# Kernel tuning notes

Measured on AMD Instinct MI355X. Metric: run time of the kernel, lower is better.

The kernel has to match this reference:

```python
import jax, jax.numpy as jnp
import numpy as np

B = 8192
C, S1, S2 = 3, 64, 64
F = C * S1 * S2          # 12288 flattened input features
SU = 4096                # s_units
HID = 1024               # hidden_size
NL = 4                   # s_layers
D = 8                    # num_domains
H1, H2, NW = 28, 14, 5   # omniglot head dims, num_ways
BN_EPS = 1e-5
LEAK = 0.001


def setup_inputs() -> dict:
    key = jax.random.key(0)
    ks = jax.random.split(key, 24)
    sc = 0.02
    n = lambda k, shp: (jax.random.normal(k, shp, jnp.float32) * sc)
    return {
        'x_s': jax.random.normal(ks[0], (B, C, S1, S2), jnp.float32),
        'x_p': jax.random.normal(ks[1], (B, C, S1, S2), jnp.float32),
        'tt': jax.random.randint(ks[2], (B,), 0, D),
        'domain_id': 3,
        # Shared MLP
        'W_in': n(ks[3], (F, SU)),  'b_in': jnp.zeros((SU,), jnp.float32),
        'W_hid': n(ks[4], (SU, SU)), 'b_hid': jnp.zeros((SU,), jnp.float32),
        'W_out': n(ks[5], (SU, HID)), 'b_out': jnp.zeros((HID,), jnp.float32),
        # Private per-domain linear (stacked)
        'Wp': n(ks[6], (D, F, HID)), 'bp': jnp.zeros((D, HID), jnp.float32),
        # BatchNorm1d affine params
        'gamma': jnp.ones((2 * HID,), jnp.float32),
        'beta': jnp.zeros((2 * HID,), jnp.float32),
        # Per-domain head MLPs (stacked)
        'Wh1': n(ks[7], (D, 2 * HID, H1)), 'bh1': jnp.zeros((D, H1), jnp.float32),
        'Wh2': n(ks[8], (D, H1, H2)),      'bh2': jnp.zeros((D, H2), jnp.float32),
        'Wh3': n(ks[9], (D, H2, NW)),      'bh3': jnp.zeros((D, NW), jnp.float32),
    }


def _forward(x_s, x_p, tt, domain_id, W_in, b_in, W_hid, b_hid, W_out, b_out,
             Wp, bp, gamma, beta, Wh1, bh1, Wh2, bh2, Wh3, bh3):
    b = x_s.shape[0]
    hs = x_s.reshape(b, -1)
    hp = x_p.reshape(b, -1)

    # Shared branch (dropout = identity in eval)
    h = jax.nn.relu(hs @ W_in + b_in)
    for _ in range(NL):
        h = jax.nn.relu(h @ W_hid + b_hid)
    h_shared = jax.nn.relu(h @ W_out + b_out)

    # Private branch: single domain-selected linear + LeakyReLU(0.001)
    h_priv = jax.nn.leaky_relu(hp @ Wp[domain_id] + bp[domain_id], LEAK)

    x = jnp.concatenate([h_shared, h_priv], axis=1)  # [B, 2*HID]

    # BatchNorm1d (training-mode batch statistics, biased variance)
    mean = jnp.mean(x, axis=0)
    var = jnp.var(x, axis=0)
    x = (x - mean) * jax.lax.rsqrt(var + BN_EPS) * gamma + beta

    # Per-sample task-routed heads: gather weights by tt, batched GEMMs
    y = jax.nn.relu(jnp.einsum('bf,bfo->bo', x, Wh1[tt]) + bh1[tt])
    y = jax.nn.relu(jnp.einsum('bf,bfo->bo', y, Wh2[tt]) + bh2[tt])
    y = jnp.einsum('bf,bfo->bo', y, Wh3[tt]) + bh3[tt]
    return y  # [B, num_ways]


def reference(x_s, x_p, tt, domain_id, W_in, b_in, W_hid, b_hid, W_out, b_out,
              Wp, bp, gamma, beta, Wh1, bh1, Wh2, bh2, Wh3, bh3):
    return _forward(x_s, x_p, tt, domain_id, W_in, b_in, W_hid, b_hid,
                    W_out, b_out, Wp, bp, gamma, beta,
                    Wh1, bh1, Wh2, bh2, Wh3, bh3)
```

## Files before the change

### kernel.cpp

```cpp
#include <hip/hip_runtime.h>
#include <hip/hip_bf16.h>

#define BQ    8192
#define FIN   12288
#define SUN   4096
#define HIDN  1024
#define XW    2048
#define H1N   28
#define H2N   14
#define NWAY  5
#define BN_EPS 1e-5f
#define LEAKS 0.001f

typedef __bf16 bf16x8 __attribute__((ext_vector_type(8)));
typedef float  f32x4  __attribute__((ext_vector_type(4)));
typedef unsigned short ushort8 __attribute__((ext_vector_type(8)));

__device__ __forceinline__ unsigned short f2bf(float f) {
    unsigned u = __float_as_uint(f);
    unsigned r = u + 0x7fffu + ((u >> 16) & 1u);
    return (unsigned short)(r >> 16);
}

__device__ __forceinline__ ushort8 cvt8(const float4 a, const float4 b) {
    union { __bf16 h[8]; ushort8 u; } r;
    r.h[0] = (__bf16)a.x; r.h[1] = (__bf16)a.y;
    r.h[2] = (__bf16)a.z; r.h[3] = (__bf16)a.w;
    r.h[4] = (__bf16)b.x; r.h[5] = (__bf16)b.y;
    r.h[6] = (__bf16)b.z; r.h[7] = (__bf16)b.w;
    return r.u;
}

#define TO_LDS(p) ((__attribute__((address_space(3))) void*)(p))
#define TO_GLB(p) ((const __attribute__((address_space(1))) void*)(p))


__global__ __launch_bounds__(256) void cvt_bf16(
    const float* __restrict__ in, unsigned short* __restrict__ out, long long n8)
{
    const long long idx = (long long)blockIdx.x * 256 + threadIdx.x;
    const long long stride = (long long)gridDim.x * 256;
    for (long long i = idx; i < n8; i += stride) {
        const float4 a = ((const float4*)in)[2 * i];
        const float4 b = ((const float4*)in)[2 * i + 1];
        ((ushort8*)out)[i] = cvt8(a, b);
    }
}

__global__ __launch_bounds__(256) void transpose_cvt(
    const float* __restrict__ in, unsigned short* __restrict__ out,
    int R, int Cc, const int* __restrict__ dom)
{
    if (dom) in += (size_t)(*dom) * (size_t)R * (size_t)Cc;
    __shared__ float tile[64][65];
    const int t  = threadIdx.x;
    const int tr = t >> 4;
    const int tc = t & 15;
    const int c0 = blockIdx.x * 64;
    const int r0 = blockIdx.y * 64;

    #pragma unroll
    for (int q = 0; q < 4; ++q) {
        const int r = r0 + tr + q * 16;
        const float4 v = *(const float4*)&in[(size_t)r * Cc + c0 + tc * 4];
        tile[tc*4+0][tr + q*16] = v.x;
        tile[tc*4+1][tr + q*16] = v.y;
        tile[tc*4+2][tr + q*16] = v.z;
        tile[tc*4+3][tr + q*16] = v.w;
    }
    __syncthreads();
    #pragma unroll
    for (int q = 0; q < 4; ++q) {
        const int c = c0 + tr + q * 16;
        ushort4 o;
        o.x = f2bf(tile[tr + q*16][tc*4+0]);
        o.y = f2bf(tile[tr + q*16][tc*4+1]);
        o.z = f2bf(tile[tr + q*16][tc*4+2]);
        o.w = f2bf(tile[tr + q*16][tc*4+3]);
        *(ushort4*)&out[(size_t)c * R + r0 + tc * 4] = o;
    }
}

template<bool A_F32, bool OUT_F32, int ACT>
__global__ __launch_bounds__(256) void gemm_mfma(
    const void* __restrict__ Ap, const unsigned short* __restrict__ Bt,
    const float* __restrict__ bias, void* __restrict__ Cp,
    int M, int N, int K, int ldc, int cc0,
    const int* __restrict__ dom, int biasStride)
{
    __shared__ alignas(16) unsigned short As[128 * 32];
    __shared__ alignas(16) unsigned short Bs[128 * 32];

    const int nbx = N >> 7;
    int wg = blockIdx.x;
    const int nwg = gridDim.x;
    if ((nwg & 7) == 0) {
        const int cpx = nwg >> 3;
        wg = (wg & 7) * cpx + (wg >> 3);
    }
    const int bx = wg % nbx, by = wg / nbx;
    const int row0 = by << 7, col0 = bx << 7;

    const int t  = threadIdx.x;
    const int w  = t >> 6;
    const int l  = t & 63;
    const int wr = w >> 1, wc = w & 1;
    const int lr = l & 15, lk = l >> 4;
    const int rsw = (lr >> 1) & 3;

    f32x4 acc[4][4];
    #pragma unroll
    for (int i = 0; i < 4; ++i)
        #pragma unroll
        for (int j = 0; j < 4; ++j)
            acc[i][j] = (f32x4)(0.f);

    const int srow = l >> 2;
    const int skb  = (((l & 3) ^ ((l >> 3) & 3)) * 16);
    const float* Af = (const float*)Ap;
    const unsigned short* Ab = (const unsigned short*)Ap;

    for (int k0 = 0; k0 < K; k0 += 32) {
        __syncthreads();

        #pragma unroll
        for (int c = 0; c < 2; ++c) {
            const int inst = w * 2 + c;
            const int row  = inst * 16 + srow;
            const char* src = (const char*)Bt +
                (((size_t)(col0 + row) * K + k0) * 2 + skb);
            char* dst = (char*)Bs + inst * 1024;
            __builtin_amdgcn_global_load_lds(TO_GLB(src), TO_LDS(dst), 16, 0, 0);
        }
        if (!A_F32) {
            #pragma unroll
            for (int c = 0; c < 2; ++c) {
                const int inst = w * 2 + c;
                const int row  = inst * 16 + srow;
                const char* src = (const char*)Ab +
                    (((size_t)(row0 + row) * K + k0) * 2 + skb);
                char* dst = (char*)As + inst * 1024;
                __builtin_amdgcn_global_load_lds(TO_GLB(src), TO_LDS(dst), 16, 0, 0);
            }
        } else {
            #pragma unroll
            for (int c = 0; c < 2; ++c) {
                const int ci  = t + 256 * c;
                const int row = ci >> 2;
                const int ko  = (((ci & 3) ^ ((ci >> 3) & 3)) * 8);
                const float* s = Af + (size_t)(row0 + row) * K + k0 + ko;
                const float4 v0 = *(const float4*)s;
                const float4 v1 = *(const float4*)(s + 4);
                *(ushort8*)&As[ci * 8] = cvt8(v0, v1);
            }
        }
        __syncthreads();

        bf16x8 af[4], bfv[4];
        #pragma unroll
        for (int i = 0; i < 4; ++i)
            af[i]  = *(const bf16x8*)&As[(wr*64 + i*16 + lr) * 32 + (lk ^ rsw) * 8];
        #pragma unroll
        for (int j = 0; j < 4; ++j)
            bfv[j] = *(const bf16x8*)&Bs[(wc*64 + j*16 + lr) * 32 + (lk ^ rsw) * 8];
        #pragma unroll
        for (int i = 0; i < 4; ++i)
            #pragma unroll
            for (int j = 0; j < 4; ++j)
                acc[i][j] = __builtin_amdgcn_mfma_f32_16x16x32_bf16(
                    af[i], bfv[j], acc[i][j], 0, 0, 0);
    }

    if (dom) bias += (*dom) * biasStride;
    const int colb = col0 + wc * 64 + lr;
    const int rowb = row0 + wr * 64 + lk * 4;
    float bj[4];
    #pragma unroll
    for (int j = 0; j < 4; ++j) bj[j] = bias[colb + j * 16];

    #pragma unroll
    for (int i = 0; i < 4; ++i) {
        #pragma unroll
        for (int r = 0; r < 4; ++r) {
            const size_t row = rowb + i * 16 + r;
            #pragma unroll
            for (int j = 0; j < 4; ++j) {
                float x = acc[i][j][r] + bj[j];
                if (ACT == 1)      x = fmaxf(x, 0.f);
                else if (ACT == 2) x = (x > 0.f) ? x : LEAKS * x;
                const size_t idx = row * (size_t)ldc + cc0 + colb + j * 16;
                if (OUT_F32) ((float*)Cp)[idx] = x;
                else         ((unsigned short*)Cp)[idx] = f2bf(x);
            }
        }
    }
}

__global__ __launch_bounds__(512, 2) void gemm256(
    const unsigned short* __restrict__ A, const unsigned short* __restrict__ Bt,
    const float* __restrict__ bias, unsigned short* __restrict__ C,
    int M, int N, int K)
{
    __shared__ alignas(16) unsigned short lds[3][2][256 * 32];

    const int nbx = N >> 8;
    int wg = blockIdx.x;
    const int nwg = gridDim.x;
    if ((nwg & 7) == 0) {
        const int cpx = nwg >> 3;
        wg = (wg & 7) * cpx + (wg >> 3);
    }
    const int bx = wg % nbx, by = wg / nbx;
    const int row0 = by << 8, col0 = bx << 8;

    const int t  = threadIdx.x;
    const int w  = t >> 6, l = t & 63;
    const int wr = w >> 2, wc = w & 3;
    const int lr = l & 15, lk = l >> 4;
    const int rsw = (lr >> 1) & 3;
    const int srow = l >> 2;
    const int skel = ((l & 3) ^ ((l >> 3) & 3)) * 8;

    f32x4 acc[8][4];
    #pragma unroll
    for (int i = 0; i < 8; ++i)
        #pragma unroll
        for (int j = 0; j < 4; ++j)
            acc[i][j] = (f32x4)(0.f);

    const int NT = K >> 5;

    #define STAGE256(tile_)  do {                                            \
        const int k0_  = (tile_) << 5;                                       \
        const int buf_ = (tile_) % 3;                                        \
        _Pragma("unroll")                                                    \
        for (int s_ = 0; s_ < 2; ++s_) {                                     \
            const int c_   = w * 2 + s_;                                     \
            const int row_ = c_ * 16 + srow;                                 \
            __builtin_amdgcn_global_load_lds(                                \
                TO_GLB(A + (size_t)(row0 + row_) * K + k0_ + skel),          \
                TO_LDS((char*)&lds[buf_][0][0] + c_ * 1024), 16, 0, 0);      \
            __builtin_amdgcn_global_load_lds(                                \
                TO_GLB(Bt + (size_t)(col0 + row_) * K + k0_ + skel),         \
                TO_LDS((char*)&lds[buf_][1][0] + c_ * 1024), 16, 0, 0);      \
        }                                                                    \
    } while (0)

    STAGE256(0);
    if (NT > 1) {
        STAGE256(1);
        asm volatile("s_waitcnt vmcnt(4)" ::: "memory");
    } else {
        asm volatile("s_waitcnt vmcnt(0)" ::: "memory");
    }
    __builtin_amdgcn_sched_barrier(0);
    __builtin_amdgcn_s_barrier();
    __builtin_amdgcn_sched_barrier(0);

    for (int tt = 0; tt < NT; ++tt) {
        const int buf = tt % 3;
        if (tt + 2 < NT) STAGE256(tt + 2);
        __builtin_amdgcn_sched_barrier(0);

        bf16x8 af[8], bfv[4];
        #pragma unroll
        for (int i = 0; i < 8; ++i)
            af[i]  = *(const bf16x8*)&lds[buf][0][(wr*128 + i*16 + lr) * 32 + (lk ^ rsw) * 8];
        #pragma unroll
        for (int j = 0; j < 4; ++j)
            bfv[j] = *(const bf16x8*)&lds[buf][1][(wc*64 + j*16 + lr) * 32 + (lk ^ rsw) * 8];

        __builtin_amdgcn_s_setprio(1);
        #pragma unroll
        for (int j = 0; j < 4; ++j)
            #pragma unroll
            for (int i = 0; i < 8; ++i)
                acc[i][j] = __builtin_amdgcn_mfma_f32_16x16x32_bf16(
                    af[i], bfv[j], acc[i][j], 0, 0, 0);
        __builtin_amdgcn_s_setprio(0);

        if (tt + 1 < NT) {
            if (tt + 2 < NT) asm volatile("s_waitcnt vmcnt(4)" ::: "memory");
            else             asm volatile("s_waitcnt vmcnt(0)" ::: "memory");
            __builtin_amdgcn_sched_barrier(0);
            __builtin_amdgcn_s_barrier();
            __builtin_amdgcn_sched_barrier(0);
        }
    }
    #undef STAGE256

    const int colb = col0 + wc * 64 + lr;
    const int rowb = row0 + wr * 128 + lk * 4;
    float bj[4];
    #pragma unroll
    for (int j = 0; j < 4; ++j) bj[j] = bias[colb + j * 16];

    #pragma unroll
    for (int i = 0; i < 8; ++i) {
        #pragma unroll
        for (int r = 0; r < 4; ++r) {
            const size_t row = rowb + i * 16 + r;
            #pragma unroll
            for (int j = 0; j < 4; ++j) {
                float x = fmaxf(acc[i][j][r] + bj[j], 0.f);
                C[row * (size_t)N + colb + j * 16] = f2bf(x);
            }
        }
    }
}

template<bool OUT_F32, int ACT>
__global__ __launch_bounds__(256, 2) void gemm128(
    const unsigned short* __restrict__ A, const unsigned short* __restrict__ Bt,
    const float* __restrict__ bias, void* __restrict__ Cp,
    int M, int N, int K, int ldc, int cc0,
    const int* __restrict__ dom, int biasStride)
{
    __shared__ alignas(16) unsigned short lds[3][2][128 * 32];

    const int nbx = N >> 7;
    int wg = blockIdx.x;
    const int nwg = gridDim.x;
    if ((nwg & 7) == 0) {
        const int cpx = nwg >> 3;
        wg = (wg & 7) * cpx + (wg >> 3);
    }
    const int bx = wg % nbx, by = wg / nbx;
    const int row0 = by << 7, col0 = bx << 7;

    const int t  = threadIdx.x;
    const int w  = t >> 6, l = t & 63;
    const int wr = w >> 1, wc = w & 1;
    const int lr = l & 15, lk = l >> 4;
    const int rsw = (lr >> 1) & 3;
    const int srow = l >> 2;
    const int skel = ((l & 3) ^ ((l >> 3) & 3)) * 8;

    f32x4 acc[4][4];
    #pragma unroll
    for (int i = 0; i < 4; ++i)
        #pragma unroll
        for (int j = 0; j < 4; ++j)
            acc[i][j] = (f32x4)(0.f);

    const int NT = K >> 5;

    #define STAGE128(tile_)  do {                                            \
        const int k0_  = (tile_) << 5;                                       \
        const int buf_ = (tile_) % 3;                                        \
        _Pragma("unroll")                                                    \
        for (int s_ = 0; s_ < 2; ++s_) {                                     \
            const int c_   = w * 2 + s_;                                     \
            const int row_ = c_ * 16 + srow;                                 \
            __builtin_amdgcn_global_load_lds(                                \
                TO_GLB(A + (size_t)(row0 + row_) * K + k0_ + skel),          \
                TO_LDS((char*)&lds[buf_][0][0] + c_ * 1024), 16, 0, 0);      \
            __builtin_amdgcn_global_load_lds(                                \
                TO_GLB(Bt + (size_t)(col0 + row_) * K + k0_ + skel),         \
                TO_LDS((char*)&lds[buf_][1][0] + c_ * 1024), 16, 0, 0);      \
        }                                                                    \
    } while (0)

    STAGE128(0);
    if (NT > 1) {
        STAGE128(1);
        asm volatile("s_waitcnt vmcnt(4)" ::: "memory");
    } else {
        asm volatile("s_waitcnt vmcnt(0)" ::: "memory");
    }
    __builtin_amdgcn_sched_barrier(0);
    __builtin_amdgcn_s_barrier();
    __builtin_amdgcn_sched_barrier(0);

    for (int tt = 0; tt < NT; ++tt) {
        const int buf = tt % 3;
        if (tt + 2 < NT) STAGE128(tt + 2);
        __builtin_amdgcn_sched_barrier(0);

        bf16x8 af[4], bfv[4];
        #pragma unroll
        for (int i = 0; i < 4; ++i)
            af[i]  = *(const bf16x8*)&lds[buf][0][(wr*64 + i*16 + lr) * 32 + (lk ^ rsw) * 8];
        #pragma unroll
        for (int j = 0; j < 4; ++j)
            bfv[j] = *(const bf16x8*)&lds[buf][1][(wc*64 + j*16 + lr) * 32 + (lk ^ rsw) * 8];

        #pragma unroll
        for (int j = 0; j < 4; ++j)
            #pragma unroll
            for (int i = 0; i < 4; ++i)
                acc[i][j] = __builtin_amdgcn_mfma_f32_16x16x32_bf16(
                    af[i], bfv[j], acc[i][j], 0, 0, 0);

        if (tt + 1 < NT) {
            if (tt + 2 < NT) asm volatile("s_waitcnt vmcnt(4)" ::: "memory");
            else             asm volatile("s_waitcnt vmcnt(0)" ::: "memory");
            __builtin_amdgcn_sched_barrier(0);
            __builtin_amdgcn_s_barrier();
            __builtin_amdgcn_sched_barrier(0);
        }
    }
    #undef STAGE128

    if (dom) bias += (*dom) * biasStride;
    const int colb = col0 + wc * 64 + lr;
    const int rowb = row0 + wr * 64 + lk * 4;
    float bj[4];
    #pragma unroll
    for (int j = 0; j < 4; ++j) bj[j] = bias[colb + j * 16];

    #pragma unroll
    for (int i = 0; i < 4; ++i) {
        #pragma unroll
        for (int r = 0; r < 4; ++r) {
            const size_t row = rowb + i * 16 + r;
            #pragma unroll
            for (int j = 0; j < 4; ++j) {
                float x = acc[i][j][r] + bj[j];
                if (ACT == 1)      x = fmaxf(x, 0.f);
                else if (ACT == 2) x = (x > 0.f) ? x : LEAKS * x;
                const size_t idx = row * (size_t)ldc + cc0 + colb + j * 16;
                if (OUT_F32) ((float*)Cp)[idx] = x;
                else         ((unsigned short*)Cp)[idx] = f2bf(x);
            }
        }
    }
}

__global__ __launch_bounds__(256) void bn_stats_a(
    const float* __restrict__ X, float* __restrict__ psum, float* __restrict__ pss)
{
    const int c  = blockIdx.x * 256 + threadIdx.x;
    const int rb = blockIdx.y;
    float s = 0.f, ss = 0.f;
    const int r0 = rb * 256;
    for (int r = r0; r < r0 + 256; ++r) {
        float v = X[(size_t)r * XW + c];
        s += v; ss = fmaf(v, v, ss);
    }
    psum[rb * XW + c] = s;
    pss [rb * XW + c] = ss;
}

__global__ __launch_bounds__(256) void bn_stats_b(
    const float* __restrict__ psum, const float* __restrict__ pss,
    const float* __restrict__ gamma, const float* __restrict__ beta,
    float* __restrict__ scale, float* __restrict__ shift)
{
    const int c = blockIdx.x * 256 + threadIdx.x;
    float s = 0.f, ss = 0.f;
    for (int rb = 0; rb < 32; ++rb) { s += psum[rb * XW + c]; ss += pss[rb * XW + c]; }
    const float inv = 1.f / (float)BQ;
    const float mean = s * inv;
    const float var  = ss * inv - mean * mean;
    const float sc = gamma[c] * rsqrtf(var + BN_EPS);
    scale[c] = sc;
    shift[c] = beta[c] - mean * sc;
}

__global__ __launch_bounds__(256) void head_kernel(
    const float* __restrict__ X, const float* __restrict__ scale,
    const float* __restrict__ shift, const int* __restrict__ tt,
    const float* __restrict__ Wh1, const float* __restrict__ bh1,
    const float* __restrict__ Wh2, const float* __restrict__ bh2,
    const float* __restrict__ Wh3, const float* __restrict__ bh3,
    float* __restrict__ out)
{
    __shared__ float xs[4][XW];
    __shared__ float y1[4][H1N];
    __shared__ float y2[4][H2N + 2];

    const int t = threadIdx.x;
    const int w = t >> 6;
    const int l = t & 63;
    const int s = blockIdx.x * 4 + w;
    const int d = tt[s];

    #pragma unroll 4
    for (int i = 0; i < XW / 64; ++i) {
        const int c = i * 64 + l;
        xs[w][c] = fmaf(X[(size_t)s * XW + c], scale[c], shift[c]);
    }
    __syncthreads();

    if (l < H1N) {
        const float* W1 = Wh1 + (size_t)d * XW * H1N;
        float acc = bh1[d * H1N + l];
        #pragma unroll 8
        for (int c = 0; c < XW; ++c)
            acc = fmaf(xs[w][c], W1[c * H1N + l], acc);
        y1[w][l] = fmaxf(acc, 0.f);
    }
    __syncthreads();

    if (l < H2N) {
        const float* W2 = Wh2 + (size_t)d * H1N * H2N;
        float acc = bh2[d * H2N + l];
        #pragma unroll
        for (int c = 0; c < H1N; ++c)
            acc = fmaf(y1[w][c], W2[c * H2N + l], acc);
        y2[w][l] = fmaxf(acc, 0.f);
    }
    __syncthreads();

    if (l < NWAY) {
        const float* W3 = Wh3 + (size_t)d * H2N * NWAY;
        float acc = bh3[d * NWAY + l];
        #pragma unroll
        for (int c = 0; c < H2N; ++c)
            acc = fmaf(y2[w][c], W3[c * NWAY + l], acc);
        out[(size_t)s * NWAY + l] = acc;
    }
}

extern "C" void kernel_launch(void* const* d_in, const int* in_sizes, int n_in,
                              void* d_out, int out_size, void* d_ws, size_t ws_size,
                              hipStream_t stream)
{
    const float* x_s   = (const float*)d_in[0];
    const float* x_p   = (const float*)d_in[1];
    const int*   tt    = (const int*)  d_in[2];
    const int*   dom   = (const int*)  d_in[3];
    const float* W_in  = (const float*)d_in[4];
    const float* b_in  = (const float*)d_in[5];
    const float* W_hid = (const float*)d_in[6];
    const float* b_hid = (const float*)d_in[7];
    const float* W_out = (const float*)d_in[8];
    const float* b_out = (const float*)d_in[9];
    const float* Wp    = (const float*)d_in[10];
    const float* bp    = (const float*)d_in[11];
    const float* gamma = (const float*)d_in[12];
    const float* beta  = (const float*)d_in[13];
    const float* Wh1   = (const float*)d_in[14];
    const float* bh1   = (const float*)d_in[15];
    const float* Wh2   = (const float*)d_in[16];
    const float* bh2   = (const float*)d_in[17];
    const float* Wh3   = (const float*)d_in[18];
    const float* bh3   = (const float*)d_in[19];
    float* out = (float*)d_out;

    const dim3 blk(256);
    char* w = (char*)d_ws;

    const size_t FAST_NEED = 470810624ull;

    if (ws_size >= FAST_NEED) {
        unsigned short* xb    = (unsigned short*)w;
        unsigned short* WinT  = (unsigned short*)(w + 201326592);
        unsigned short* WoutT = (unsigned short*)(w + 201326592);
        unsigned short* WpT   = (unsigned short*)(w + 209715200);
        unsigned short* actA  = (unsigned short*)(w + 301989888);
        unsigned short* actB  = (unsigned short*)(w + 369098752);
        float*          X     = (float*)(w + 369098752);
        unsigned short* WhidT = (unsigned short*)(w + 436207616);
        float*          psum  = (float*)(w + 469762048);
        float*          pss   = psum + 32 * XW;
        float*          scale = pss  + 32 * XW;
        float*          shift = scale + XW;

        cvt_bf16<<<dim3(2048), blk, 0, stream>>>(x_s, xb, (long long)BQ * FIN / 8);
        transpose_cvt<<<dim3(SUN/64,  FIN/64), blk, 0, stream>>>(W_in,  WinT,  FIN, SUN,  nullptr);
        transpose_cvt<<<dim3(SUN/64,  SUN/64), blk, 0, stream>>>(W_hid, WhidT, SUN, SUN,  nullptr);

        gemm256<<<dim3(512), dim3(512), 0, stream>>>(xb, WinT, b_in, actA, BQ, SUN, FIN);

        transpose_cvt<<<dim3(HIDN/64, SUN/64), blk, 0, stream>>>(W_out, WoutT, SUN, HIDN, nullptr);
        transpose_cvt<<<dim3(HIDN/64, FIN/64), blk, 0, stream>>>(Wp,    WpT,   FIN, HIDN, dom);
        cvt_bf16<<<dim3(2048), blk, 0, stream>>>(x_p, xb, (long long)BQ * FIN / 8);

        gemm256<<<dim3(512), dim3(512), 0, stream>>>(actA, WhidT, b_hid, actB, BQ, SUN, SUN);
        gemm256<<<dim3(512), dim3(512), 0, stream>>>(actB, WhidT, b_hid, actA, BQ, SUN, SUN);
        gemm256<<<dim3(512), dim3(512), 0, stream>>>(actA, WhidT, b_hid, actB, BQ, SUN, SUN);
        gemm256<<<dim3(512), dim3(512), 0, stream>>>(actB, WhidT, b_hid, actA, BQ, SUN, SUN);

        gemm128<true,1><<<dim3(512), blk, 0, stream>>>(
            actA, WoutT, b_out, X, BQ, HIDN, SUN, XW, 0, nullptr, 0);
        gemm128<true,2><<<dim3(512), blk, 0, stream>>>(
            xb, WpT, bp, X, BQ, HIDN, FIN, XW, HIDN, dom, HIDN);

        bn_stats_a<<<dim3(XW/256, 32), blk, 0, stream>>>(X, psum, pss);
        bn_stats_b<<<dim3(XW/256),     blk, 0, stream>>>(psum, pss, gamma, beta, scale, shift);
        head_kernel<<<dim3(BQ/4), blk, 0, stream>>>(X, scale, shift, tt,
                                                    Wh1, bh1, Wh2, bh2, Wh3, bh3, out);
        return;
    }

    unsigned short* actA  = (unsigned short*)w;
    unsigned short* actB  = (unsigned short*)(w + 67108864);
    float*          X     = (float*)(w + 67108864);
    unsigned short* WinT  = (unsigned short*)(w + 134217728);
    unsigned short* WoutT = (unsigned short*)(w + 134217728);
    unsigned short* WpT   = (unsigned short*)(w + 142606336);
    float*          psum  = (float*)(w + 167772160);
    float*          pss   = psum + 32 * XW;
    float*          scale = pss  + 32 * XW;
    float*          shift = scale + XW;
    unsigned short* WhidT = (unsigned short*)(w + 234881024);

    transpose_cvt<<<dim3(SUN/64,  FIN/64), blk, 0, stream>>>(W_in,  WinT,  FIN, SUN,  nullptr);
    transpose_cvt<<<dim3(SUN/64,  SUN/64), blk, 0, stream>>>(W_hid, WhidT, SUN, SUN,  nullptr);

    gemm_mfma<true,false,1><<<dim3(2048), blk, 0, stream>>>(
        x_s, WinT, b_in, actA, BQ, SUN, FIN, SUN, 0, nullptr, 0);

    transpose_cvt<<<dim3(HIDN/64, SUN/64), blk, 0, stream>>>(W_out, WoutT, SUN, HIDN, nullptr);
    transpose_cvt<<<dim3(HIDN/64, FIN/64), blk, 0, stream>>>(Wp,    WpT,   FIN, HIDN, dom);

    gemm256<<<dim3(512), dim3(512), 0, stream>>>(actA, WhidT, b_hid, actB, BQ, SUN, SUN);
    gemm256<<<dim3(512), dim3(512), 0, stream>>>(actB, WhidT, b_hid, actA, BQ, SUN, SUN);
    gemm256<<<dim3(512), dim3(512), 0, stream>>>(actA, WhidT, b_hid, actB, BQ, SUN, SUN);
    gemm256<<<dim3(512), dim3(512), 0, stream>>>(actB, WhidT, b_hid, actA, BQ, SUN, SUN);

    gemm128<true,1><<<dim3(512), blk, 0, stream>>>(
        actA, WoutT, b_out, X, BQ, HIDN, SUN, XW, 0, nullptr, 0);
    gemm_mfma<true,true,2><<<dim3(512), blk, 0, stream>>>(
        x_p, WpT, bp, X, BQ, HIDN, FIN, XW, HIDN, dom, HIDN);

    bn_stats_a<<<dim3(XW/256, 32), blk, 0, stream>>>(X, psum, pss);
    bn_stats_b<<<dim3(XW/256),     blk, 0, stream>>>(psum, pss, gamma, beta, scale, shift);
    head_kernel<<<dim3(BQ/4), blk, 0, stream>>>(X, scale, shift, tt,
                                                Wh1, bh1, Wh2, bh2, Wh3, bh3, out);
}
```

Before: 2.521 ms.

## Rework 256x256 GEMM to BK=64 double buffer with phased MFMA scheduling

Replaces the 3-stage BK=32 LDS pipeline with a 2-stage BK=64 double buffer using an XOR swizzle over 8 chunks. The inner loop is split into four quadrant phases that interleave LDS reads with MFMAs. An optional PHASED variant adds workgroup barriers around each phase so waves issue their MFMA bursts together, and it is applied to alternating hidden-layer GEMMs. The aim is fewer barriers per K and better LDS/MFMA overlap. The cost is that each prefetch now waits on vmcnt(0), so there is less latency hiding, and LDS usage per block rises to 128KB.

```diff
diff --git a/kernel.cpp b/kernel.cpp
--- a/kernel.cpp
+++ b/kernel.cpp
@@ -34,7 +34,6 @@
 #define TO_LDS(p) ((__attribute__((address_space(3))) void*)(p))
 #define TO_GLB(p) ((const __attribute__((address_space(1))) void*)(p))
 
-
 __global__ __launch_bounds__(256) void cvt_bf16(
     const float* __restrict__ in, unsigned short* __restrict__ out, long long n8)
 {
@@ -196,12 +195,14 @@
     }
 }
 
-__global__ __launch_bounds__(512, 2) void gemm256(
+template<bool PHASED>
+__global__ __launch_bounds__(512, 2) void gemm256v2(
     const unsigned short* __restrict__ A, const unsigned short* __restrict__ Bt,
     const float* __restrict__ bias, unsigned short* __restrict__ C,
     int M, int N, int K)
 {
-    __shared__ alignas(16) unsigned short lds[3][2][256 * 32];
+    __shared__ alignas(16) unsigned short As[2][256 * 64];
+    __shared__ alignas(16) unsigned short Bs[2][256 * 64];
 
     const int nbx = N >> 8;
     int wg = blockIdx.x;
@@ -217,9 +218,6 @@
     const int w  = t >> 6, l = t & 63;
     const int wr = w >> 2, wc = w & 3;
     const int lr = l & 15, lk = l >> 4;
-    const int rsw = (lr >> 1) & 3;
-    const int srow = l >> 2;
-    const int skel = ((l & 3) ^ ((l >> 3) & 3)) * 8;
 
     f32x4 acc[8][4];
     #pragma unroll
@@ -228,66 +226,86 @@
         for (int j = 0; j < 4; ++j)
             acc[i][j] = (f32x4)(0.f);
 
-    const int NT = K >> 5;
-
-    #define STAGE256(tile_)  do {                                            \
-        const int k0_  = (tile_) << 5;                                       \
-        const int buf_ = (tile_) % 3;                                        \
-        _Pragma("unroll")                                                    \
-        for (int s_ = 0; s_ < 2; ++s_) {                                     \
-            const int c_   = w * 2 + s_;                                     \
-            const int row_ = c_ * 16 + srow;                                 \
-            __builtin_amdgcn_global_load_lds(                                \
-                TO_GLB(A + (size_t)(row0 + row_) * K + k0_ + skel),          \
-                TO_LDS((char*)&lds[buf_][0][0] + c_ * 1024), 16, 0, 0);      \
-            __builtin_amdgcn_global_load_lds(                                \
-                TO_GLB(Bt + (size_t)(col0 + row_) * K + k0_ + skel),         \
-                TO_LDS((char*)&lds[buf_][1][0] + c_ * 1024), 16, 0, 0);      \
-        }                                                                    \
+    const int NT = K >> 6;
+
+    #define STAGEV2(tile_)  do {                                              \
+        const int k0_ = (tile_) << 6;                                         \
+        const int b_  = (tile_) & 1;                                          \
+        _Pragma("unroll")                                                     \
+        for (int h_ = 0; h_ < 2; ++h_)                                        \
+        _Pragma("unroll")                                                     \
+        for (int s_ = 0; s_ < 2; ++s_) {                                      \
+            const int ch_  = h_ * 1024 + s_ * 512 + t;                        \
+            const int row_ = ch_ >> 3;                                        \
+            const int g_   = (ch_ & 7) ^ (row_ & 7);                          \
+            __builtin_amdgcn_global_load_lds(                                 \
+                TO_GLB(A + (size_t)(row0 + row_) * K + k0_ + g_ * 8),         \
+                TO_LDS((char*)&As[b_][0] + ch_ * 16), 16, 0, 0);              \
+            __builtin_amdgcn_global_load_lds(                                 \
+                TO_GLB(Bt + (size_t)(col0 + row_) * K + k0_ + g_ * 8),        \
+                TO_LDS((char*)&Bs[b_][0] + ch_ * 16), 16, 0, 0);              \
+        }                                                                     \
     } while (0)
 
-    STAGE256(0);
-    if (NT > 1) {
-        STAGE256(1);
-        asm volatile("s_waitcnt vmcnt(4)" ::: "memory");
-    } else {
-        asm volatile("s_waitcnt vmcnt(0)" ::: "memory");
-    }
+    STAGEV2(0);
+    asm volatile("s_waitcnt vmcnt(0)" ::: "memory");
     __builtin_amdgcn_sched_barrier(0);
     __builtin_amdgcn_s_barrier();
     __builtin_amdgcn_sched_barrier(0);
 
     for (int tt = 0; tt < NT; ++tt) {
-        const int buf = tt % 3;
-        if (tt + 2 < NT) STAGE256(tt + 2);
+        const int b = tt & 1;
+        if (tt + 1 < NT) STAGEV2(tt + 1);
         __builtin_amdgcn_sched_barrier(0);
 
-        bf16x8 af[8], bfv[4];
-        #pragma unroll
-        for (int i = 0; i < 8; ++i)
-            af[i]  = *(const bf16x8*)&lds[buf][0][(wr*128 + i*16 + lr) * 32 + (lk ^ rsw) * 8];
-        #pragma unroll
-        for (int j = 0; j < 4; ++j)
-            bfv[j] = *(const bf16x8*)&lds[buf][1][(wc*64 + j*16 + lr) * 32 + (lk ^ rsw) * 8];
-
-        __builtin_amdgcn_s_setprio(1);
-        #pragma unroll
-        for (int j = 0; j < 4; ++j)
-            #pragma unroll
-            for (int i = 0; i < 8; ++i)
-                acc[i][j] = __builtin_amdgcn_mfma_f32_16x16x32_bf16(
-                    af[i], bfv[j], acc[i][j], 0, 0, 0);
-        __builtin_amdgcn_s_setprio(0);
+        #pragma unroll
+        for (int ph = 0; ph < 4; ++ph) {
+            const int qi = ph >> 1, qj = ph & 1;
+
+            bf16x8 av[2][4], bv[2][2];
+            #pragma unroll
+            for (int ks = 0; ks < 2; ++ks)
+                #pragma unroll
+                for (int i = 0; i < 4; ++i) {
+                    const int row = wr * 128 + qi * 64 + i * 16 + lr;
+                    av[ks][i] = *(const bf16x8*)
+                        &As[b][row * 64 + (((ks * 4 + lk) ^ (row & 7)) << 3)];
+                }
+            #pragma unroll
+            for (int ks = 0; ks < 2; ++ks)
+                #pragma unroll
+                for (int j = 0; j < 2; ++j) {
+                    const int row = wc * 64 + qj * 32 + j * 16 + lr;
+                    bv[ks][j] = *(const bf16x8*)
+                        &Bs[b][row * 64 + (((ks * 4 + lk) ^ (row & 7)) << 3)];
+                }
+
+            if (PHASED) {
+                __builtin_amdgcn_s_barrier();
+                asm volatile("s_waitcnt lgkmcnt(0)" ::: "memory");
+                __builtin_amdgcn_sched_barrier(0);
+            }
+            __builtin_amdgcn_s_setprio(1);
+            #pragma unroll
+            for (int ks = 0; ks < 2; ++ks)
+                #pragma unroll
+                for (int j = 0; j < 2; ++j)
+                    #pragma unroll
+                    for (int i = 0; i < 4; ++i)
+                        acc[qi*4+i][qj*2+j] = __builtin_amdgcn_mfma_f32_16x16x32_bf16(
+                            av[ks][i], bv[ks][j], acc[qi*4+i][qj*2+j], 0, 0, 0);
+            __builtin_amdgcn_s_setprio(0);
+            if (PHASED) __builtin_amdgcn_s_barrier();
+        }
 
         if (tt + 1 < NT) {
-            if (tt + 2 < NT) asm volatile("s_waitcnt vmcnt(4)" ::: "memory");
-            else             asm volatile("s_waitcnt vmcnt(0)" ::: "memory");
+            asm volatile("s_waitcnt vmcnt(0)" ::: "memory");
             __builtin_amdgcn_sched_barrier(0);
             __builtin_amdgcn_s_barrier();
             __builtin_amdgcn_sched_barrier(0);
         }
     }
-    #undef STAGE256
+    #undef STAGEV2
 
     const int colb = col0 + wc * 64 + lr;
     const int rowb = row0 + wr * 128 + lk * 4;
@@ -562,16 +580,16 @@
         transpose_cvt<<<dim3(SUN/64,  FIN/64), blk, 0, stream>>>(W_in,  WinT,  FIN, SUN,  nullptr);
         transpose_cvt<<<dim3(SUN/64,  SUN/64), blk, 0, stream>>>(W_hid, WhidT, SUN, SUN,  nullptr);
 
-        gemm256<<<dim3(512), dim3(512), 0, stream>>>(xb, WinT, b_in, actA, BQ, SUN, FIN);
+        gemm256v2<false><<<dim3(512), dim3(512), 0, stream>>>(xb, WinT, b_in, actA, BQ, SUN, FIN);
 
         transpose_cvt<<<dim3(HIDN/64, SUN/64), blk, 0, stream>>>(W_out, WoutT, SUN, HIDN, nullptr);
         transpose_cvt<<<dim3(HIDN/64, FIN/64), blk, 0, stream>>>(Wp,    WpT,   FIN, HIDN, dom);
         cvt_bf16<<<dim3(2048), blk, 0, stream>>>(x_p, xb, (long long)BQ * FIN / 8);
 
-        gemm256<<<dim3(512), dim3(512), 0, stream>>>(actA, WhidT, b_hid, actB, BQ, SUN, SUN);
-        gemm256<<<dim3(512), dim3(512), 0, stream>>>(actB, WhidT, b_hid, actA, BQ, SUN, SUN);
-        gemm256<<<dim3(512), dim3(512), 0, stream>>>(actA, WhidT, b_hid, actB, BQ, SUN, SUN);
-        gemm256<<<dim3(512), dim3(512), 0, stream>>>(actB, WhidT, b_hid, actA, BQ, SUN, SUN);
+        gemm256v2<false><<<dim3(512), dim3(512), 0, stream>>>(actA, WhidT, b_hid, actB, BQ, SUN, SUN);
+        gemm256v2<true ><<<dim3(512), dim3(512), 0, stream>>>(actB, WhidT, b_hid, actA, BQ, SUN, SUN);
+        gemm256v2<false><<<dim3(512), dim3(512), 0, stream>>>(actA, WhidT, b_hid, actB, BQ, SUN, SUN);
+        gemm256v2<true ><<<dim3(512), dim3(512), 0, stream>>>(actB, WhidT, b_hid, actA, BQ, SUN, SUN);
 
         gemm128<true,1><<<dim3(512), blk, 0, stream>>>(
             actA, WoutT, b_out, X, BQ, HIDN, SUN, XW, 0, nullptr, 0);
@@ -606,10 +624,10 @@
     transpose_cvt<<<dim3(HIDN/64, SUN/64), blk, 0, stream>>>(W_out, WoutT, SUN, HIDN, nullptr);
     transpose_cvt<<<dim3(HIDN/64, FIN/64), blk, 0, stream>>>(Wp,    WpT,   FIN, HIDN, dom);
 
-    gemm256<<<dim3(512), dim3(512), 0, stream>>>(actA, WhidT, b_hid, actB, BQ, SUN, SUN);
-    gemm256<<<dim3(512), dim3(512), 0, stream>>>(actB, WhidT, b_hid, actA, BQ, SUN, SUN);
-    gemm256<<<dim3(512), dim3(512), 0, stream>>>(actA, WhidT, b_hid, actB, BQ, SUN, SUN);
-    gemm256<<<dim3(512), dim3(512), 0, stream>>>(actB, WhidT, b_hid, actA, BQ, SUN, SUN);
+    gemm256v2<false><<<dim3(512), dim3(512), 0, stream>>>(actA, WhidT, b_hid, actB, BQ, SUN, SUN);
+    gemm256v2<false><<<dim3(512), dim3(512), 0, stream>>>(actB, WhidT, b_hid, actA, BQ, SUN, SUN);
+    gemm256v2<false><<<dim3(512), dim3(512), 0, stream>>>(actA, WhidT, b_hid, actB, BQ, SUN, SUN);
+    gemm256v2<false><<<dim3(512), dim3(512), 0, stream>>>(actB, WhidT, b_hid, actA, BQ, SUN, SUN);
 
     gemm128<true,1><<<dim3(512), blk, 0, stream>>>(
         actA, WoutT, b_out, X, BQ, HIDN, SUN, XW, 0, nullptr, 0);
```

New measurement: 3.058 ms. +21.3%, slower.

## Add 8-phase pipelined 256x256 GEMM variant for two hidden layers

Applied to the files above, without the earlier changes.

Adds a new 256x256-tile bf16 MFMA GEMM kernel that splits each pair of 64-deep K tiles into eight phases. Each phase issues LDS reads and global-to-LDS loads for upcoming quarter tiles and interleaves them with 16-MFMA bursts, using barriers and setprio. The aim is to hide memory and LDS latency behind matrix math. It is used for only two of the four hidden-layer GEMMs, alternating with the old kernel, which looks like an A/B comparison. The scheme also brings a barrier on every phase and tight vmcnt bookkeeping.

```diff
diff --git a/kernel.cpp b/kernel.cpp
--- a/kernel.cpp
+++ b/kernel.cpp
@@ -33,7 +33,6 @@
 
 #define TO_LDS(p) ((__attribute__((address_space(3))) void*)(p))
 #define TO_GLB(p) ((const __attribute__((address_space(1))) void*)(p))
-
 
 __global__ __launch_bounds__(256) void cvt_bf16(
     const float* __restrict__ in, unsigned short* __restrict__ out, long long n8)
@@ -304,6 +303,158 @@
             for (int j = 0; j < 4; ++j) {
                 float x = fmaxf(acc[i][j][r] + bj[j], 0.f);
                 C[row * (size_t)N + colb + j * 16] = f2bf(x);
+            }
+        }
+    }
+}
+
+__global__ __launch_bounds__(512, 2) void gemm256_8ph(
+    const unsigned short* __restrict__ A, const unsigned short* __restrict__ Bt,
+    const float* __restrict__ bias, unsigned short* __restrict__ C,
+    int M, int N, int K)
+{
+    __shared__ alignas(16) unsigned short lds[2][2][2][128 * 64];
+
+    const int nbx = N >> 8;
+    int wg = blockIdx.x;
+    const int nwg = gridDim.x;
+    if ((nwg & 7) == 0) { const int cpx = nwg >> 3; wg = (wg & 7) * cpx + (wg >> 3); }
+    const int bx = wg % nbx, by = wg / nbx;
+    const int row0 = by << 8, col0 = bx << 8;
+
+    const int t = threadIdx.x;
+    const int w = t >> 6, l = t & 63;
+    const int wr = w >> 2, wc = w & 3;
+    const int lr = l & 15, lk = l >> 4;
+
+    f32x4 acc[8][4];
+    #pragma unroll
+    for (int i = 0; i < 8; ++i)
+        #pragma unroll
+        for (int j = 0; j < 4; ++j) acc[i][j] = (f32x4)(0.f);
+
+    const int NT = K >> 6;
+    const int NI = NT >> 1;
+
+    #define STG(mat_, kt_, h_) do {                                              \
+        const unsigned short* gb_ = (mat_) ? Bt : A;                              \
+        const int gr0_ = (mat_) ? col0 : row0;                                    \
+        _Pragma("unroll")                                                         \
+        for (int s_ = 0; s_ < 2; ++s_) {                                          \
+            const int c_   = s_ * 8 + w;                                          \
+            const int row_ = c_ * 8 + (l >> 3);                                   \
+            const int g_   = (l & 7) ^ (row_ & 7);                                \
+            __builtin_amdgcn_global_load_lds(                                     \
+                TO_GLB(gb_ + (size_t)(gr0_ + (h_) * 128 + row_) * K + (kt_) * 64 + g_ * 8), \
+                TO_LDS((char*)&lds[mat_][(kt_) & 1][h_][0] + c_ * 1024), 16, 0, 0);\
+        } } while (0)
+
+    #define RD_A(dst_, buf_, qi_) do {                                            \
+        _Pragma("unroll")                                                         \
+        for (int ks_ = 0; ks_ < 2; ++ks_)                                         \
+        _Pragma("unroll")                                                         \
+        for (int ii_ = 0; ii_ < 4; ++ii_) {                                       \
+            const int rh_ = wr * 64 + ii_ * 16 + lr;                              \
+            dst_[ks_][ii_] = *(const bf16x8*)                                     \
+                &lds[0][buf_][qi_][rh_ * 64 + (((ks_ * 4 + lk) ^ (rh_ & 7)) << 3)]; \
+        } } while (0)
+
+    #define RD_B(dst_, buf_, qj_) do {                                            \
+        _Pragma("unroll")                                                         \
+        for (int ks_ = 0; ks_ < 2; ++ks_)                                         \
+        _Pragma("unroll")                                                         \
+        for (int jj_ = 0; jj_ < 2; ++jj_) {                                       \
+            const int rh_ = wc * 32 + jj_ * 16 + lr;                              \
+            dst_[ks_][jj_] = *(const bf16x8*)                                     \
+                &lds[1][buf_][qj_][rh_ * 64 + (((ks_ * 4 + lk) ^ (rh_ & 7)) << 3)]; \
+        } } while (0)
+
+    #define SYNC_IN() do {                                                        \
+        __builtin_amdgcn_sched_barrier(0);                                        \
+        __builtin_amdgcn_s_barrier();                                             \
+        asm volatile("s_waitcnt lgkmcnt(0)" ::: "memory");                        \
+        __builtin_amdgcn_sched_barrier(0); } while (0)
+
+    #define MFMA16(aa_, bb_, qi_, qj_) do {                                       \
+        __builtin_amdgcn_s_setprio(1);                                            \
+        _Pragma("unroll")                                                         \
+        for (int ks_ = 0; ks_ < 2; ++ks_)                                         \
+        _Pragma("unroll")                                                         \
+        for (int jj_ = 0; jj_ < 2; ++jj_)                                         \
+        _Pragma("unroll")                                                         \
+        for (int ii_ = 0; ii_ < 4; ++ii_)                                         \
+            acc[(qi_)*4+ii_][(qj_)*2+jj_] = __builtin_amdgcn_mfma_f32_16x16x32_bf16( \
+                aa_[ks_][ii_], bb_[ks_][jj_], acc[(qi_)*4+ii_][(qj_)*2+jj_], 0, 0, 0); \
+        __builtin_amdgcn_s_setprio(0); } while (0)
+
+    #define PH_END() do {                                                         \
+        __builtin_amdgcn_sched_barrier(0);                                        \
+        __builtin_amdgcn_s_barrier(); } while (0)
+
+    STG(0, 0, 0); STG(0, 0, 1); STG(1, 0, 0); STG(1, 0, 1);
+    STG(0, 1, 0); STG(1, 1, 0);
+    asm volatile("s_waitcnt vmcnt(4)" ::: "memory");
+    __builtin_amdgcn_sched_barrier(0);
+    __builtin_amdgcn_s_barrier();
+    __builtin_amdgcn_sched_barrier(0);
+
+    for (int m = 0; m < NI; ++m) {
+        const int t1 = 2 * m + 1, u0 = 2 * m + 2, u1 = 2 * m + 3;
+        const bool last = (m == NI - 1);
+        bf16x8 a_[2][4], b0_[2][2], b1_[2][2];
+
+        RD_A(a_, 0, 0); RD_B(b0_, 0, 0);
+        STG(0, t1, 1);
+        SYNC_IN(); MFMA16(a_, b0_, 0, 0); PH_END();
+        RD_B(b1_, 0, 1);
+        STG(1, t1, 1);
+        SYNC_IN(); MFMA16(a_, b1_, 0, 1); PH_END();
+        RD_A(a_, 0, 1);
+        if (u0 < NT) STG(0, u0, 0);
+        SYNC_IN(); MFMA16(a_, b0_, 1, 0); PH_END();
+        if (u0 < NT) STG(1, u0, 0);
+        SYNC_IN(); MFMA16(a_, b1_, 1, 1);
+        if (last) asm volatile("s_waitcnt vmcnt(0)" ::: "memory");
+        else      asm volatile("s_waitcnt vmcnt(4)" ::: "memory");
+        PH_END();
+        RD_A(a_, 1, 0); RD_B(b0_, 1, 0);
+        if (u0 < NT) STG(0, u0, 1);
+        SYNC_IN(); MFMA16(a_, b0_, 0, 0); PH_END();
+        RD_B(b1_, 1, 1);
+        if (u0 < NT) STG(1, u0, 1);
+        SYNC_IN(); MFMA16(a_, b1_, 0, 1); PH_END();
+        RD_A(a_, 1, 1);
+        if (u1 < NT) STG(0, u1, 0);
+        SYNC_IN(); MFMA16(a_, b0_, 1, 0); PH_END();
+        if (u1 < NT) STG(1, u1, 0);
+        SYNC_IN(); MFMA16(a_, b1_, 1, 1);
+        if (!last) asm volatile("s_waitcnt vmcnt(4)" ::: "memory");
+        PH_END();
+    }
+    #undef STG
+    #undef RD_A
+    #undef RD_B
+    #undef SYNC_IN
+    #undef MFMA16
+    #undef PH_END
+
+    const int colb = col0 + wc * 32 + lr;
+    const int rowb = row0 + wr * 64 + lk * 4;
+    float bj[4];
+    #pragma unroll
+    for (int j = 0; j < 4; ++j)
+        bj[j] = bias[colb + (j >> 1) * 128 + (j & 1) * 16];
+
+    #pragma unroll
+    for (int i = 0; i < 8; ++i) {
+        const int gri = rowb + (i >> 2) * 128 + (i & 3) * 16;
+        #pragma unroll
+        for (int r = 0; r < 4; ++r) {
+            const size_t row = gri + r;
+            #pragma unroll
+            for (int j = 0; j < 4; ++j) {
+                float x = fmaxf(acc[i][j][r] + bj[j], 0.f);
+                C[row * (size_t)N + colb + (j >> 1) * 128 + (j & 1) * 16] = f2bf(x);
             }
         }
     }
@@ -568,10 +719,10 @@
         transpose_cvt<<<dim3(HIDN/64, FIN/64), blk, 0, stream>>>(Wp,    WpT,   FIN, HIDN, dom);
         cvt_bf16<<<dim3(2048), blk, 0, stream>>>(x_p, xb, (long long)BQ * FIN / 8);
 
-        gemm256<<<dim3(512), dim3(512), 0, stream>>>(actA, WhidT, b_hid, actB, BQ, SUN, SUN);
-        gemm256<<<dim3(512), dim3(512), 0, stream>>>(actB, WhidT, b_hid, actA, BQ, SUN, SUN);
-        gemm256<<<dim3(512), dim3(512), 0, stream>>>(actA, WhidT, b_hid, actB, BQ, SUN, SUN);
-        gemm256<<<dim3(512), dim3(512), 0, stream>>>(actB, WhidT, b_hid, actA, BQ, SUN, SUN);
+        gemm256_8ph<<<dim3(512), dim3(512), 0, stream>>>(actA, WhidT, b_hid, actB, BQ, SUN, SUN);
+        gemm256    <<<dim3(512), dim3(512), 0, stream>>>(actB, WhidT, b_hid, actA, BQ, SUN, SUN);
+        gemm256_8ph<<<dim3(512), dim3(512), 0, stream>>>(actA, WhidT, b_hid, actB, BQ, SUN, SUN);
+        gemm256    <<<dim3(512), dim3(512), 0, stream>>>(actB, WhidT, b_hid, actA, BQ, SUN, SUN);
 
         gemm128<true,1><<<dim3(512), blk, 0, stream>>>(
             actA, WoutT, b_out, X, BQ, HIDN, SUN, XW, 0, nullptr, 0);
```

Result: no change. 2.487 ms (-1.4%).
